# Kernel optimization log

Hardware: AMD Instinct MI355X
Metric: run time of the kernel (lower is better)

Reference implementation:

```python
import jax, jax.numpy as jnp
import numpy as np

VOCAB = 50265
EMBED = 256
HEADS = 4
HEAD_DIM = EMBED // HEADS
WINDOW = 64
NUM_CLASS = 20
B, S = 8, 2048


def setup_inputs() -> dict:
    key = jax.random.key(0)
    ks = jax.random.split(key, 12)
    sd = 0.02
    return {
        "text": jax.random.randint(ks[0], (B, S), 0, VOCAB),
        "emb": jax.random.normal(ks[1], (VOCAB, EMBED), jnp.float32) * sd,
        "in_proj_w": jax.random.normal(ks[2], (3 * EMBED, EMBED), jnp.float32) * sd,
        "in_proj_b": jnp.zeros((3 * EMBED,), jnp.float32),
        "out_proj_w": jax.random.normal(ks[3], (EMBED, EMBED), jnp.float32) * sd,
        "out_proj_b": jnp.zeros((EMBED,), jnp.float32),
        "fc1_w": jax.random.normal(ks[4], (512, EMBED), jnp.float32) * sd,
        "fc1_b": jnp.zeros((512,), jnp.float32),
        "fc2_w": jax.random.normal(ks[5], (256, 512), jnp.float32) * sd,
        "fc2_b": jnp.zeros((256,), jnp.float32),
        "fc3_w": jax.random.normal(ks[6], (NUM_CLASS, 256), jnp.float32) * sd,
        "fc3_b": jnp.zeros((NUM_CLASS,), jnp.float32),
    }


def reference(text, emb, in_proj_w, in_proj_b, out_proj_w, out_proj_b,
              fc1_w, fc1_b, fc2_w, fc2_b, fc3_w, fc3_b):
    # embedding (dropout is identity in eval mode)
    x = emb[text]  # [B,S,E]
    # fused qkv projection, as in nn.MultiheadAttention
    qkv = x @ in_proj_w.T + in_proj_b  # [B,S,3E]
    q, k, v = jnp.split(qkv, 3, axis=-1)
    q = q.reshape(B, S, HEADS, HEAD_DIM) * (1.0 / np.sqrt(HEAD_DIM))
    k = k.reshape(B, S, HEADS, HEAD_DIM)
    v = v.reshape(B, S, HEADS, HEAD_DIM)
    # banded mask: row i attends to [i-W, i+W]
    idx = jnp.arange(S)
    band = jnp.abs(idx[:, None] - idx[None, :]) <= WINDOW  # [S,S]
    scores = jnp.einsum('bqhd,bkhd->bhqk', q, k)
    scores = jnp.where(band[None, None], scores, -jnp.inf)
    attn = jax.nn.softmax(scores, axis=-1)
    out = jnp.einsum('bhqk,bkhd->bqhd', attn, v).reshape(B, S, EMBED)
    out = out @ out_proj_w.T + out_proj_b  # [B,S,E]
    # max-pool over sequence
    ctx = jnp.max(out, axis=1)  # [B,E]
    h1 = jax.nn.leaky_relu(ctx @ fc1_w.T + fc1_b, 0.01)
    h2 = jax.nn.leaky_relu(h1 @ fc2_w.T + fc2_b, 0.01)
    return h2 @ fc3_w.T + fc3_b  # [B,num_class]
```

## Files before the change

### kernel.cpp

```cpp
#include <hip/hip_runtime.h>
#include <math.h>

typedef __attribute__((ext_vector_type(4))) float f32x4;
typedef __attribute__((ext_vector_type(8))) short short8;

__device__ __forceinline__ ushort bf16r(float f) {
    unsigned u = __float_as_uint(f);
    return (ushort)((u + 0x7FFFu + ((u >> 16) & 1u)) >> 16);
}
__device__ __forceinline__ unsigned pack2(float lo, float hi) {
    return (unsigned)bf16r(lo) | ((unsigned)bf16r(hi) << 16);
}

#define GLOAD16(gp, lp)                                                        \
    __builtin_amdgcn_global_load_lds(                                          \
        (const __attribute__((address_space(1))) unsigned*)(gp),               \
        (__attribute__((address_space(3))) unsigned*)(lp), 16, 0, 0)

__global__ __launch_bounds__(256) void k_prep(
    const int* __restrict__ text, const float* __restrict__ emb,
    const float* __restrict__ ipw, const float* __restrict__ opw,
    ushort* __restrict__ Xb, ushort* __restrict__ Wqb, ushort* __restrict__ Wob)
{
    int t = blockIdx.x * 256 + threadIdx.x;
#pragma unroll
    for (int i = t; i < 1114112; i += 278528) {
        const float* src; ushort* dst;
        if (i < 1048576) {
            int row = i >> 6, f4 = i & 63;
            int tok = text[row];
            src = &emb[(size_t)tok * 256 + f4 * 4];
            dst = &Xb[(size_t)row * 256 + f4 * 4];
        } else if (i < 1097728) {
            int j = i - 1048576;
            src = &ipw[(size_t)j * 4];
            dst = &Wqb[(size_t)j * 4];
        } else {
            int j = i - 1097728;
            src = &opw[(size_t)j * 4];
            dst = &Wob[(size_t)j * 4];
        }
        float4 x = *(const float4*)src;
        uint2 pk = make_uint2(pack2(x.x, x.y), pack2(x.z, x.w));
        *(uint2*)dst = pk;
    }
}

__global__ __launch_bounds__(256) void k_qkv(
    const ushort* __restrict__ Xb, const ushort* __restrict__ Wqb,
    const float* __restrict__ bias,
    ushort* __restrict__ Qb, ushort* __restrict__ Kb, ushort* __restrict__ VTb)
{
    extern __shared__ ushort lds[];
    const int tid = threadIdx.x;
    const int lane = tid & 63, wv = tid >> 6;
    const int g = lane >> 4, c = lane & 15;
    const int wm = wv >> 1, wn = wv & 1;
    const int m0 = blockIdx.x * 128, n0 = blockIdx.y * 128;

    const int lrow = lane >> 3;
    const int lch  = lane & 7;

    f32x4 acc[4][4];
#pragma unroll
    for (int mi = 0; mi < 4; ++mi)
#pragma unroll
        for (int ni = 0; ni < 4; ++ni) acc[mi][ni] = (f32x4){0.f, 0.f, 0.f, 0.f};

#define STAGE_QKV(buf, ki)                                                     \
    {                                                                          \
        const int k0_ = (ki) * 64;                                             \
        ushort* Ad_ = lds + (buf) * 8192;                                      \
        ushort* Bd_ = lds + 16384 + (buf) * 8192;                              \
        _Pragma("unroll")                                                      \
        for (int i_ = 0; i_ < 4; ++i_) {                                       \
            int r0_ = wv * 32 + i_ * 8;                                        \
            int row_ = r0_ + lrow;                                             \
            int ch_ = lch ^ (row_ & 7);                                        \
            GLOAD16(&Xb[(size_t)(m0 + row_) * 256 + k0_ + ch_ * 8],            \
                    &Ad_[r0_ * 64]);                                           \
            GLOAD16(&Wqb[(size_t)(n0 + row_) * 256 + k0_ + ch_ * 8],           \
                    &Bd_[r0_ * 64]);                                           \
        }                                                                      \
    }

    STAGE_QKV(0, 0)
    __syncthreads();
    int cur = 0;
    for (int ki = 0; ki < 4; ++ki) {
        if (ki < 3) STAGE_QKV(cur ^ 1, ki + 1)
        const ushort* A = lds + cur * 8192;
        const ushort* B = lds + 16384 + cur * 8192;
#pragma unroll
        for (int ks = 0; ks < 2; ++ks) {
            const int ko = ks * 32 + g * 8;
            short8 am[4], bn[4];
#pragma unroll
            for (int mi = 0; mi < 4; ++mi) {
                int row = wm * 64 + mi * 16 + c;
                am[mi] = *(const short8*)&A[row * 64 + (ko ^ ((row & 7) << 3))];
            }
#pragma unroll
            for (int ni = 0; ni < 4; ++ni) {
                int row = wn * 64 + ni * 16 + c;
                bn[ni] = *(const short8*)&B[row * 64 + (ko ^ ((row & 7) << 3))];
            }
#pragma unroll
            for (int mi = 0; mi < 4; ++mi)
#pragma unroll
                for (int ni = 0; ni < 4; ++ni)
                    acc[mi][ni] = __builtin_amdgcn_mfma_f32_16x16x32_bf16(
                        am[mi], bn[ni], acc[mi][ni], 0, 0, 0);
        }
        __syncthreads();
        cur ^= 1;
    }

    const int sec = n0 >> 8;
    if (sec < 2) {
        ushort* dst = sec == 0 ? Qb : Kb;
        const float scale = sec == 0 ? 0.125f : 1.0f;
#pragma unroll
        for (int ni = 0; ni < 4; ++ni) {
            int n = n0 + wn * 64 + ni * 16 + c;
            float bv = bias[n];
            int h = (n >> 6) & 3, d = n & 63;
#pragma unroll
            for (int mi = 0; mi < 4; ++mi)
#pragma unroll
                for (int r = 0; r < 4; ++r) {
                    int m = m0 + wm * 64 + mi * 16 + g * 4 + r;
                    int bb = m >> 11, s = m & 2047;
                    dst[(size_t)((bb * 4 + h) * 2048 + s) * 64 + d] =
                        bf16r((acc[mi][ni][r] + bv) * scale);
                }
        }
    } else {
#pragma unroll
        for (int ni = 0; ni < 4; ++ni) {
            int n = n0 + wn * 64 + ni * 16 + c;
            float bv = bias[n];
            int h = (n >> 6) & 3, d = n & 63;
#pragma unroll
            for (int mi = 0; mi < 4; ++mi) {
                int sb = m0 + wm * 64 + mi * 16 + g * 4;
                int bb = sb >> 11, s = sb & 2047;
                float v0 = acc[mi][ni][0] + bv, v1 = acc[mi][ni][1] + bv;
                float v2 = acc[mi][ni][2] + bv, v3 = acc[mi][ni][3] + bv;
                uint2 pk = make_uint2(pack2(v0, v1), pack2(v2, v3));
                *(uint2*)&VTb[(size_t)((bb * 4 + h) * 64 + d) * 2048 + s] = pk;
            }
        }
    }
}

__global__ __launch_bounds__(256) void k_attn(
    const ushort* __restrict__ Qb, const ushort* __restrict__ Kb,
    const ushort* __restrict__ VTb, ushort* __restrict__ AOb)
{
    __shared__ ushort smem[29184];
    ushort* Qsm = smem;
    ushort* Ksm = smem + 4096;
    ushort* Vts = smem + 16384;
    ushort* Psm = smem;

    const int tid = threadIdx.x;
    const int lane = tid & 63, w = tid >> 6;
    const int g = lane >> 4, c = lane & 15;
    const int s0 = blockIdx.x * 64;
    const int h = blockIdx.y, b = blockIdx.z;
    const int bh = b * 4 + h;
    const size_t base = (size_t)bh * 2048 * 64;

#pragma unroll
    for (int it = 0; it < 2; ++it) {
        int ch = it * 256 + tid;
        int row = ch >> 3, c8 = ch & 7;
        uint4 v = *(const uint4*)&Qb[base + (size_t)(s0 + row) * 64 + c8 * 8];
        *(uint4*)&Qsm[row * 64 + ((c8 * 8) ^ ((row & 7) << 3))] = v;
    }
#pragma unroll
    for (int it = 0; it < 6; ++it) {
        int ch = it * 256 + tid;
        int row = ch >> 3, c8 = ch & 7;
        int ks = s0 - 64 + row;
        ks = ks < 0 ? 0 : (ks > 2047 ? 2047 : ks);
        uint4 v = *(const uint4*)&Kb[base + (size_t)ks * 64 + c8 * 8];
        *(uint4*)&Ksm[row * 64 + ((c8 * 8) ^ ((row & 7) << 3))] = v;
    }
#pragma unroll
    for (int it = 0; it < 6; ++it) {
        int d = tid >> 2, c8 = it * 4 + (tid & 3);
        const ushort* vrow = VTb + (size_t)(bh * 64 + d) * 2048;
        uint4 v = *(const uint4*)&vrow[s0 - 64 + c8 * 8];
        *(uint4*)&Vts[d * 200 + c8 * 8] = v;
    }
    __syncthreads();

    const int qrow = (w << 4) | c;
    const int swzq = (qrow & 7) << 3;
    short8 a0 = *(const short8*)&Qsm[qrow * 64 + ((g * 8) ^ swzq)];
    short8 a1 = *(const short8*)&Qsm[qrow * 64 + ((32 + g * 8) ^ swzq)];
    f32x4 accS[12];
#pragma unroll
    for (int ni = 0; ni < 12; ++ni) accS[ni] = (f32x4){0.f, 0.f, 0.f, 0.f};
#pragma unroll
    for (int ni = 0; ni < 12; ++ni) {
        int krow = ni * 16 + c;
        int swzk = (krow & 7) << 3;
        short8 b0 = *(const short8*)&Ksm[krow * 64 + ((g * 8) ^ swzk)];
        short8 b1 = *(const short8*)&Ksm[krow * 64 + ((32 + g * 8) ^ swzk)];
        accS[ni] = __builtin_amdgcn_mfma_f32_16x16x32_bf16(a0, b0, accS[ni], 0, 0, 0);
        accS[ni] = __builtin_amdgcn_mfma_f32_16x16x32_bf16(a1, b1, accS[ni], 0, 0, 0);
    }
    __syncthreads();

    float mx[4] = {-1e30f, -1e30f, -1e30f, -1e30f};
#pragma unroll
    for (int ni = 0; ni < 12; ++ni) {
        int j = ni * 16 + c;
        bool inr = (unsigned)(s0 - 64 + j) < 2048u;
#pragma unroll
        for (int r = 0; r < 4; ++r) {
            int qq = (w << 4) + g * 4 + r;
            bool valid = inr && (j >= qq) && (j <= qq + 128);
            float sv = valid ? accS[ni][r] : -1e30f;
            accS[ni][r] = sv;
            mx[r] = fmaxf(mx[r], sv);
        }
    }
#pragma unroll
    for (int hop = 1; hop <= 8; hop <<= 1)
#pragma unroll
        for (int r = 0; r < 4; ++r) mx[r] = fmaxf(mx[r], __shfl_xor(mx[r], hop));
    float L[4] = {0.f, 0.f, 0.f, 0.f};
#pragma unroll
    for (int ni = 0; ni < 12; ++ni)
#pragma unroll
        for (int r = 0; r < 4; ++r) {
            float e = __expf(accS[ni][r] - mx[r]);
            accS[ni][r] = e;
            L[r] += e;
        }
#pragma unroll
    for (int hop = 1; hop <= 8; hop <<= 1)
#pragma unroll
        for (int r = 0; r < 4; ++r) L[r] += __shfl_xor(L[r], hop);
    float inv[4];
#pragma unroll
    for (int r = 0; r < 4; ++r) inv[r] = 1.f / L[r];

#pragma unroll
    for (int ni = 0; ni < 12; ++ni)
#pragma unroll
        for (int r = 0; r < 4; ++r)
            Psm[((w << 4) + g * 4 + r) * 200 + ni * 16 + c] = bf16r(accS[ni][r]);
    __syncthreads();

    f32x4 o[4];
#pragma unroll
    for (int ni = 0; ni < 4; ++ni) o[ni] = (f32x4){0.f, 0.f, 0.f, 0.f};
    const int prow = (w << 4) | c;
#pragma unroll
    for (int jt = 0; jt < 6; ++jt) {
        short8 am = *(const short8*)&Psm[prow * 200 + jt * 32 + g * 8];
#pragma unroll
        for (int ni = 0; ni < 4; ++ni) {
            short8 bn = *(const short8*)&Vts[(ni * 16 + c) * 200 + jt * 32 + g * 8];
            o[ni] = __builtin_amdgcn_mfma_f32_16x16x32_bf16(am, bn, o[ni], 0, 0, 0);
        }
    }
#pragma unroll
    for (int ni = 0; ni < 4; ++ni)
#pragma unroll
        for (int r = 0; r < 4; ++r) {
            int q = (w << 4) + g * 4 + r;
            int d = ni * 16 + c;
            AOb[((size_t)b * 2048 + s0 + q) * 256 + h * 64 + d] =
                bf16r(o[ni][r] * inv[r]);
        }
}

__global__ __launch_bounds__(256) void k_oproj(
    const ushort* __restrict__ AOb, const ushort* __restrict__ Wob,
    const float* __restrict__ bias, unsigned* __restrict__ CTX)
{
    extern __shared__ ushort lds[];
    const int tid = threadIdx.x;
    const int lane = tid & 63, wv = tid >> 6;
    const int g = lane >> 4, c = lane & 15;
    const int wm = wv >> 1, wn = wv & 1;
    const int m0 = blockIdx.x * 128, n0 = blockIdx.y * 128;
    const int lrow = lane >> 3, lch = lane & 7;

    f32x4 acc[4][4];
#pragma unroll
    for (int mi = 0; mi < 4; ++mi)
#pragma unroll
        for (int ni = 0; ni < 4; ++ni) acc[mi][ni] = (f32x4){0.f, 0.f, 0.f, 0.f};

#define STAGE_OP(buf, ki)                                                      \
    {                                                                          \
        const int k0_ = (ki) * 64;                                             \
        ushort* Ad_ = lds + (buf) * 8192;                                      \
        ushort* Bd_ = lds + 16384 + (buf) * 8192;                              \
        _Pragma("unroll")                                                      \
        for (int i_ = 0; i_ < 4; ++i_) {                                       \
            int r0_ = wv * 32 + i_ * 8;                                        \
            int row_ = r0_ + lrow;                                             \
            int ch_ = lch ^ (row_ & 7);                                        \
            GLOAD16(&AOb[(size_t)(m0 + row_) * 256 + k0_ + ch_ * 8],           \
                    &Ad_[r0_ * 64]);                                           \
            GLOAD16(&Wob[(size_t)(n0 + row_) * 256 + k0_ + ch_ * 8],           \
                    &Bd_[r0_ * 64]);                                           \
        }                                                                      \
    }

    STAGE_OP(0, 0)
    __syncthreads();
    int cur = 0;
    for (int ki = 0; ki < 4; ++ki) {
        if (ki < 3) STAGE_OP(cur ^ 1, ki + 1)
        const ushort* A = lds + cur * 8192;
        const ushort* B = lds + 16384 + cur * 8192;
#pragma unroll
        for (int ks = 0; ks < 2; ++ks) {
            const int ko = ks * 32 + g * 8;
            short8 am[4], bn[4];
#pragma unroll
            for (int mi = 0; mi < 4; ++mi) {
                int row = wm * 64 + mi * 16 + c;
                am[mi] = *(const short8*)&A[row * 64 + (ko ^ ((row & 7) << 3))];
            }
#pragma unroll
            for (int ni = 0; ni < 4; ++ni) {
                int row = wn * 64 + ni * 16 + c;
                bn[ni] = *(const short8*)&B[row * 64 + (ko ^ ((row & 7) << 3))];
            }
#pragma unroll
            for (int mi = 0; mi < 4; ++mi)
#pragma unroll
                for (int ni = 0; ni < 4; ++ni)
                    acc[mi][ni] = __builtin_amdgcn_mfma_f32_16x16x32_bf16(
                        am[mi], bn[ni], acc[mi][ni], 0, 0, 0);
        }
        __syncthreads();
        cur ^= 1;
    }

    const int bidx = m0 >> 11;
#pragma unroll
    for (int ni = 0; ni < 4; ++ni) {
        int n = n0 + wn * 64 + ni * 16 + c;
        float mxv = -1e30f;
#pragma unroll
        for (int mi = 0; mi < 4; ++mi)
#pragma unroll
            for (int r = 0; r < 4; ++r) mxv = fmaxf(mxv, acc[mi][ni][r]);
        mxv += bias[n];
        mxv = fmaxf(mxv, __shfl_xor(mxv, 16));
        mxv = fmaxf(mxv, __shfl_xor(mxv, 32));
        if (lane < 16) {
            unsigned bits = __float_as_uint(mxv);
            unsigned en = (bits & 0x80000000u) ? ~bits : (bits | 0x80000000u);
            atomicMax(&CTX[bidx * 256 + n], en);
        }
    }
}

__global__ __launch_bounds__(256) void k_fc1(
    const unsigned* __restrict__ CTX, const float* __restrict__ w,
    const float* __restrict__ bias, float* __restrict__ H1)
{
    __shared__ float cs[256];
    const int tid = threadIdx.x;
    const int row = blockIdx.x >> 1, half = blockIdx.x & 1;
    unsigned u = CTX[row * 256 + tid];
    unsigned bits = (u & 0x80000000u) ? (u & 0x7fffffffu) : ~u;
    cs[tid] = __uint_as_float(bits);
    __syncthreads();
    const int o = half * 256 + tid;
    float a = bias[o];
#pragma unroll 8
    for (int c4 = 0; c4 < 64; ++c4) {
        float4 w4 = *(const float4*)&w[o * 256 + c4 * 4];
        a = fmaf(w4.x, cs[c4 * 4 + 0], a);
        a = fmaf(w4.y, cs[c4 * 4 + 1], a);
        a = fmaf(w4.z, cs[c4 * 4 + 2], a);
        a = fmaf(w4.w, cs[c4 * 4 + 3], a);
    }
    H1[row * 512 + o] = a > 0.f ? a : 0.01f * a;
}

__global__ __launch_bounds__(256) void k_head(
    const float* __restrict__ H1, const float* __restrict__ w2,
    const float* __restrict__ b2, const float* __restrict__ w3,
    const float* __restrict__ b3, float* __restrict__ out)
{
    __shared__ float H1s[8][516];
    __shared__ float H2s[8][260];
    const int tid = threadIdx.x;
    for (int i = tid; i < 4096; i += 256) H1s[i >> 9][i & 511] = H1[i];
    __syncthreads();
    float a2[8];
#pragma unroll
    for (int r = 0; r < 8; ++r) a2[r] = b2[tid];
    for (int c4 = 0; c4 < 128; ++c4) {
        float4 w4 = *(const float4*)&w2[tid * 512 + c4 * 4];
#pragma unroll
        for (int r = 0; r < 8; ++r) {
            a2[r] = fmaf(w4.x, H1s[r][c4 * 4 + 0], a2[r]);
            a2[r] = fmaf(w4.y, H1s[r][c4 * 4 + 1], a2[r]);
            a2[r] = fmaf(w4.z, H1s[r][c4 * 4 + 2], a2[r]);
            a2[r] = fmaf(w4.w, H1s[r][c4 * 4 + 3], a2[r]);
        }
    }
#pragma unroll
    for (int r = 0; r < 8; ++r) {
        float v = a2[r];
        H2s[r][tid] = v > 0.f ? v : 0.01f * v;
    }
    __syncthreads();
    if (tid < 160) {
        int r = tid / 20, o = tid % 20;
        float a = b3[o];
#pragma unroll 8
        for (int c4 = 0; c4 < 64; ++c4) {
            float4 w4 = *(const float4*)&w3[o * 256 + c4 * 4];
            a = fmaf(w4.x, H2s[r][c4 * 4 + 0], a);
            a = fmaf(w4.y, H2s[r][c4 * 4 + 1], a);
            a = fmaf(w4.z, H2s[r][c4 * 4 + 2], a);
            a = fmaf(w4.w, H2s[r][c4 * 4 + 3], a);
        }
        out[tid] = a;
    }
}

extern "C" void kernel_launch(void* const* d_in, const int* in_sizes, int n_in,
                              void* d_out, int out_size, void* d_ws, size_t ws_size,
                              hipStream_t stream)
{
    (void)in_sizes; (void)n_in; (void)out_size; (void)ws_size;
    const int*   text = (const int*)d_in[0];
    const float* emb  = (const float*)d_in[1];
    const float* ipw  = (const float*)d_in[2];
    const float* ipb  = (const float*)d_in[3];
    const float* opw  = (const float*)d_in[4];
    const float* opb  = (const float*)d_in[5];
    const float* f1w  = (const float*)d_in[6];
    const float* f1b  = (const float*)d_in[7];
    const float* f2w  = (const float*)d_in[8];
    const float* f2b  = (const float*)d_in[9];
    const float* f3w  = (const float*)d_in[10];
    const float* f3b  = (const float*)d_in[11];
    float* out = (float*)d_out;

    unsigned char* w8 = (unsigned char*)d_ws;
    ushort* Xb  = (ushort*)(w8);
    ushort* Qb  = (ushort*)(w8 + 8388608);
    ushort* Kb  = (ushort*)(w8 + 16777216);
    ushort* VTb = (ushort*)(w8 + 25165824);
    ushort* AOb = (ushort*)(w8 + 33619968);
    ushort* Wqb = (ushort*)(w8 + 42008576);
    ushort* Wob = (ushort*)(w8 + 42401792);
    unsigned* CTX = (unsigned*)(w8 + 42532864);
    float* H1 = (float*)(w8 + 42541056);

    hipFuncSetAttribute((const void*)k_qkv,
                        hipFuncAttributeMaxDynamicSharedMemorySize, 65536);
    hipFuncSetAttribute((const void*)k_oproj,
                        hipFuncAttributeMaxDynamicSharedMemorySize, 65536);

    hipMemsetAsync(CTX, 0, 8192, stream);
    k_prep<<<1088, 256, 0, stream>>>(text, emb, ipw, opw, Xb, Wqb, Wob);
    k_qkv<<<dim3(128, 6), 256, 65536, stream>>>(Xb, Wqb, ipb, Qb, Kb, VTb);
    k_attn<<<dim3(32, 4, 8), 256, 0, stream>>>(Qb, Kb, VTb, AOb);
    k_oproj<<<dim3(128, 2), 256, 65536, stream>>>(AOb, Wob, opb, CTX);
    k_fc1<<<16, 256, 0, stream>>>(CTX, f1w, f1b, H1);
    k_head<<<1, 256, 0, stream>>>(H1, f2w, f2b, f3w, f3b, out);
}
```

Measured before the change: 195.8 us.

## Split MLP head into parallel fc1/fc2/fc3 kernels with split-K shuffle reductions

The single-block fc2+fc3 head kernel is split so that fc2 runs over 64 blocks, with eight lanes per output doing split-K work and combining their partial sums through shuffles. fc1 likewise moves from 16 to 64 blocks using a four-way split-K. The aim is to remove the serial bottleneck of one block streaming the entire 512x256 fc2 weight matrix. The cost is one extra kernel launch and an H2 round trip through global memory.

```diff
diff --git a/kernel.cpp b/kernel.cpp
--- a/kernel.cpp
+++ b/kernel.cpp
@@ -57,7 +57,6 @@
     const int g = lane >> 4, c = lane & 15;
     const int wm = wv >> 1, wn = wv & 1;
     const int m0 = blockIdx.x * 128, n0 = blockIdx.y * 128;
-
     const int lrow = lane >> 3;
     const int lch  = lane & 7;
 
@@ -374,63 +373,78 @@
 {
     __shared__ float cs[256];
     const int tid = threadIdx.x;
-    const int row = blockIdx.x >> 1, half = blockIdx.x & 1;
+    const int row = blockIdx.x >> 3, chunk = blockIdx.x & 7;
     unsigned u = CTX[row * 256 + tid];
     unsigned bits = (u & 0x80000000u) ? (u & 0x7fffffffu) : ~u;
     cs[tid] = __uint_as_float(bits);
     __syncthreads();
-    const int o = half * 256 + tid;
-    float a = bias[o];
-#pragma unroll 8
-    for (int c4 = 0; c4 < 64; ++c4) {
-        float4 w4 = *(const float4*)&w[o * 256 + c4 * 4];
-        a = fmaf(w4.x, cs[c4 * 4 + 0], a);
-        a = fmaf(w4.y, cs[c4 * 4 + 1], a);
-        a = fmaf(w4.z, cs[c4 * 4 + 2], a);
-        a = fmaf(w4.w, cs[c4 * 4 + 3], a);
-    }
-    H1[row * 512 + o] = a > 0.f ? a : 0.01f * a;
-}
-
-__global__ __launch_bounds__(256) void k_head(
-    const float* __restrict__ H1, const float* __restrict__ w2,
-    const float* __restrict__ b2, const float* __restrict__ w3,
-    const float* __restrict__ b3, float* __restrict__ out)
-{
-    __shared__ float H1s[8][516];
-    __shared__ float H2s[8][260];
-    const int tid = threadIdx.x;
-    for (int i = tid; i < 4096; i += 256) H1s[i >> 9][i & 511] = H1[i];
-    __syncthreads();
-    float a2[8];
-#pragma unroll
-    for (int r = 0; r < 8; ++r) a2[r] = b2[tid];
-    for (int c4 = 0; c4 < 128; ++c4) {
-        float4 w4 = *(const float4*)&w2[tid * 512 + c4 * 4];
-#pragma unroll
-        for (int r = 0; r < 8; ++r) {
-            a2[r] = fmaf(w4.x, H1s[r][c4 * 4 + 0], a2[r]);
-            a2[r] = fmaf(w4.y, H1s[r][c4 * 4 + 1], a2[r]);
-            a2[r] = fmaf(w4.z, H1s[r][c4 * 4 + 2], a2[r]);
-            a2[r] = fmaf(w4.w, H1s[r][c4 * 4 + 3], a2[r]);
-        }
-    }
-#pragma unroll
-    for (int r = 0; r < 8; ++r) {
-        float v = a2[r];
-        H2s[r][tid] = v > 0.f ? v : 0.01f * v;
-    }
+    const int o = chunk * 64 + (tid >> 2);
+    const int k0 = (tid & 3) * 64;
+    float a = 0.f;
+#pragma unroll 16
+    for (int i = 0; i < 16; ++i) {
+        float4 w4 = *(const float4*)&w[o * 256 + k0 + i * 4];
+        a = fmaf(w4.x, cs[k0 + i * 4 + 0], a);
+        a = fmaf(w4.y, cs[k0 + i * 4 + 1], a);
+        a = fmaf(w4.z, cs[k0 + i * 4 + 2], a);
+        a = fmaf(w4.w, cs[k0 + i * 4 + 3], a);
+    }
+    a += __shfl_xor(a, 1);
+    a += __shfl_xor(a, 2);
+    if ((tid & 3) == 0) {
+        a += bias[o];
+        H1[row * 512 + o] = a > 0.f ? a : 0.01f * a;
+    }
+}
+
+__global__ __launch_bounds__(256) void k_fc2(
+    const float* __restrict__ H1, const float* __restrict__ w,
+    const float* __restrict__ bias, float* __restrict__ H2)
+{
+    __shared__ float hs[512];
+    const int tid = threadIdx.x;
+    const int row = blockIdx.x >> 3, chunk = blockIdx.x & 7;
+    hs[tid] = H1[row * 512 + tid];
+    hs[tid + 256] = H1[row * 512 + tid + 256];
+    __syncthreads();
+    const int o = chunk * 32 + (tid >> 3);
+    const int k0 = (tid & 7) * 64;
+    float a = 0.f;
+#pragma unroll 16
+    for (int i = 0; i < 16; ++i) {
+        float4 w4 = *(const float4*)&w[o * 512 + k0 + i * 4];
+        a = fmaf(w4.x, hs[k0 + i * 4 + 0], a);
+        a = fmaf(w4.y, hs[k0 + i * 4 + 1], a);
+        a = fmaf(w4.z, hs[k0 + i * 4 + 2], a);
+        a = fmaf(w4.w, hs[k0 + i * 4 + 3], a);
+    }
+    a += __shfl_xor(a, 1);
+    a += __shfl_xor(a, 2);
+    a += __shfl_xor(a, 4);
+    if ((tid & 7) == 0) {
+        a += bias[o];
+        H2[row * 256 + o] = a > 0.f ? a : 0.01f * a;
+    }
+}
+
+__global__ __launch_bounds__(256) void k_fc3(
+    const float* __restrict__ H2, const float* __restrict__ w,
+    const float* __restrict__ bias, float* __restrict__ out)
+{
+    __shared__ float hs[8][260];
+    const int tid = threadIdx.x;
+    for (int i = tid; i < 2048; i += 256) hs[i >> 8][i & 255] = H2[i];
     __syncthreads();
     if (tid < 160) {
         int r = tid / 20, o = tid % 20;
-        float a = b3[o];
+        float a = bias[o];
 #pragma unroll 8
         for (int c4 = 0; c4 < 64; ++c4) {
-            float4 w4 = *(const float4*)&w3[o * 256 + c4 * 4];
-            a = fmaf(w4.x, H2s[r][c4 * 4 + 0], a);
-            a = fmaf(w4.y, H2s[r][c4 * 4 + 1], a);
-            a = fmaf(w4.z, H2s[r][c4 * 4 + 2], a);
-            a = fmaf(w4.w, H2s[r][c4 * 4 + 3], a);
+            float4 w4 = *(const float4*)&w[o * 256 + c4 * 4];
+            a = fmaf(w4.x, hs[r][c4 * 4 + 0], a);
+            a = fmaf(w4.y, hs[r][c4 * 4 + 1], a);
+            a = fmaf(w4.z, hs[r][c4 * 4 + 2], a);
+            a = fmaf(w4.w, hs[r][c4 * 4 + 3], a);
         }
         out[tid] = a;
     }
@@ -465,6 +479,7 @@
     ushort* Wob = (ushort*)(w8 + 42401792);
     unsigned* CTX = (unsigned*)(w8 + 42532864);
     float* H1 = (float*)(w8 + 42541056);
+    float* H2 = (float*)(w8 + 42557440);
 
     hipFuncSetAttribute((const void*)k_qkv,
                         hipFuncAttributeMaxDynamicSharedMemorySize, 65536);
@@ -476,6 +491,7 @@
     k_qkv<<<dim3(128, 6), 256, 65536, stream>>>(Xb, Wqb, ipb, Qb, Kb, VTb);
     k_attn<<<dim3(32, 4, 8), 256, 0, stream>>>(Qb, Kb, VTb, AOb);
     k_oproj<<<dim3(128, 2), 256, 65536, stream>>>(AOb, Wob, opb, CTX);
-    k_fc1<<<16, 256, 0, stream>>>(CTX, f1w, f1b, H1);
-    k_head<<<1, 256, 0, stream>>>(H1, f2w, f2b, f3w, f3b, out);
-}
+    k_fc1<<<64, 256, 0, stream>>>(CTX, f1w, f1b, H1);
+    k_fc2<<<64, 256, 0, stream>>>(H1, f2w, f2b, H2);
+    k_fc3<<<1, 256, 0, stream>>>(H2, f3w, f3b, out);
+}
```

Result: faster. 161.7 us (-17.4%).
